# Performance work log

Hardware: AMD Instinct MI355X
Metric: run time of the kernel (lower is better)

## Reference

```python
import jax, jax.numpy as jnp
from jax import lax
import numpy as np

KSIZE = 25  # kernel_size init arg


def _generate_kernel(size):
    center = size // 2
    kernel = np.zeros((size, size), dtype=np.float32)
    for i in range(size):
        if i < center + 1:
            for j in range(size):
                if j < center:
                    kernel[i, j] = j - center - i
                elif j > center:
                    kernel[i, j] = -kernel[i, size - j - 1]
        elif i > center:
            kernel[i, :] = kernel[size - i - 1, :]
    return kernel


def _edge_forward(cube):
    # cube: [B, H, W, C]. Equivalent to the torch block-tiled computation:
    # zero-pad by p, for every interior pixel compute spectral-angle (SAD)
    # between the center spectrum and each pixel of its k x k neighborhood,
    # then 'convolve' (single valid k x k cross-correlation == weighted sum)
    # the SAD patch with fixed gradient kernels Kx / Ky.
    B, H, W, C = cube.shape
    k = KSIZE
    p = k // 2
    Kx = jnp.asarray(_generate_kernel(k))  # [k, k]
    Ky = Kx.T                               # rearrange 'h w -> w h'
    kx_flat = Kx.reshape(-1)
    ky_flat = Ky.reshape(-1)

    padded = jnp.pad(cube, ((0, 0), (p, p), (p, p), (0, 0)))  # [B, H+2p, W+2p, C]
    norm_pad = jnp.sqrt(jnp.sum(padded * padded, axis=-1))    # [B, H+2p, W+2p]
    center = cube                                             # center spectra
    norm_c = norm_pad[:, p:p + H, p:p + W]                    # [B, H, W]

    # Scan over the k*k window offsets; accumulate the two gradient sums
    # without ever materializing the [B,H,W,k,k] SAD volume.
    def step(carry, idx):
        gx, gy = carry
        di, dj = idx // k, idx % k
        shifted = lax.dynamic_slice(padded, (0, di, dj, 0), (B, H, W, C))
        norm_s = lax.dynamic_slice(norm_pad, (0, di, dj), (B, H, W))
        numer = jnp.einsum('bhwc,bhwc->bhw', center, shifted)
        # eps 1e-4 matches torch; tiny clip guards fp32 roundoff past +/-1
        ratio = jnp.clip(numer / (norm_c * norm_s + 1e-4), -1.0 + 1e-6, 1.0 - 1e-6)
        sad = jnp.arccos(ratio)
        return (gx + sad * kx_flat[idx], gy + sad * ky_flat[idx]), None

    init = (jnp.zeros((B, H, W), cube.dtype), jnp.zeros((B, H, W), cube.dtype))
    (gx, gy), _ = lax.scan(jax.checkpoint(step), init, jnp.arange(k * k))
    edge = jnp.abs(gx) + jnp.abs(gy)
    # the torch code zeroes a pad_len border before global-max normalization
    out = jnp.pad(edge[:, p:H - p, p:W - p], ((0, 0), (p, p), (p, p)))
    return out / jnp.max(out)


def setup_inputs() -> dict:
    key = jax.random.key(0)
    cube = jax.random.uniform(key, (1, 400, 400, 128), dtype=jnp.float32)
    return {"cube": cube}


def reference(cube):
    return _edge_forward(cube)
```

## Files before the change

### kernel.cpp

```cpp
#include <hip/hip_runtime.h>
#include <cstdint>
#include <cstddef>


typedef _Float16 half8 __attribute__((ext_vector_type(8)));
typedef float    f32x4 __attribute__((ext_vector_type(4)));

#define HW   400
#define NP   (HW*HW)
#define CCH  128
#define W16  416
#define ROWE (W16*CCH)
#define PAD  12
#define IEND 388


__device__ __forceinline__ float acos_fast(float x) {
  float ax = fabsf(x);
  float s  = __builtin_amdgcn_sqrtf(1.0f - ax);
  float p  = fmaf(ax, -0.0187292994f, 0.0742610134f);
  p = fmaf(p, ax, -0.2121143967f);
  p = fmaf(p, ax,  1.5707287572f);
  float r = s * p;
  return (x >= 0.0f) ? r : (3.14159265359f - r);
}

__global__ void cvt_kernel(const float* __restrict__ cube,
                           _Float16* __restrict__ c16,
                           unsigned* __restrict__ gmax) {
  __shared__ float part[64];
  int pg = blockIdx.x;
  int r  = blockIdx.y;
  int t  = threadIdx.x;
  if (pg == 0 && r == 0 && t == 0) *gmax = 0u;
  int i  = t & 15;
  int q  = (t >> 4) & 3;
  int ks = t >> 6;
  int px = pg*16 + i;
  float v[8];
  if (px < HW) {
    const float* src = cube + ((size_t)(r*HW + px))*CCH + ks*32 + q*8;
    #pragma unroll
    for (int j = 0; j < 8; ++j) v[j] = src[j];
  } else {
    #pragma unroll
    for (int j = 0; j < 8; ++j) v[j] = 0.f;
  }
  float ss = 0.f;
  #pragma unroll
  for (int j = 0; j < 8; ++j) ss += v[j]*v[j];
  ss += __shfl_xor(ss, 16);
  ss += __shfl_xor(ss, 32);
  if (q == 0) part[i*4 + ks] = ss;
  __syncthreads();
  f32x4 pp = *(const f32x4*)&part[i*4];
  float tot = pp.x + pp.y + pp.z + pp.w;
  float sc = (tot > 0.f) ? rsqrtf(tot) : 0.f;
  half8 hv;
  #pragma unroll
  for (int j = 0; j < 8; ++j) hv[j] = (_Float16)(v[j]*sc);
  *(half8*)(c16 + (size_t)r*ROWE + pg*2048 + t*8) = hv;
}

__global__ __launch_bounds__(64, 4) void edge_kernel(
    const _Float16* __restrict__ c16,
    float* __restrict__ gxp, float* __restrict__ gyp) {
  const int id   = blockIdx.x;
  const int g    = (id & 7)*1128 + (id >> 3);
  const int gh   = g / 24;
  const int rem  = g - gh*24;
  const int h    = gh + PAD;
  const int wb   = rem >> 1;
  const int half = rem & 1;
  const int l  = threadIdx.x;
  const int c  = l & 15, q = l >> 4;
  const int w0 = PAD + 32*wb;
  const int g0 = 2*wb;

  half8 A[2][4];
  #pragma unroll
  for (int t = 0; t < 2; ++t) {
    int px = w0 + 16*t + c;
    const _Float16* p = c16 + (size_t)h*ROWE + (px >> 4)*2048 + q*128 + (px & 15)*8;
    #pragma unroll
    for (int ks = 0; ks < 4; ++ks)
      A[t][ks] = *(const half8*)(p + ks*512);
  }

  const float cq = (float)(c - 4*q);

  float gx[2][4], gy[2][4];
  #pragma unroll
  for (int t = 0; t < 2; ++t)
    #pragma unroll
    for (int rr = 0; rr < 4; ++rr) { gx[t][rr] = 0.f; gy[t][rr] = 0.f; }

  const _Float16* bBase = c16 + g0*2048 + (size_t)l*8;
  const int diLo = half ? 13 : 0;
  const int diHi = half ? 25 : 13;

  #pragma unroll 1
  for (int di = diLo; di < diHi; ++di) {
    const int r = h + di - PAD;
    const _Float16* rowB = bBase + (size_t)r*ROWE;

    f32x4 acc[2][3];
    #pragma unroll
    for (int t = 0; t < 2; ++t)
      #pragma unroll
      for (int d = 0; d < 3; ++d) acc[t][d] = (f32x4){0.f,0.f,0.f,0.f};

    #pragma unroll
    for (int ks = 0; ks < 4; ++ks) {
      half8 B0 = *(const half8*)(rowB + 0*2048 + ks*512);
      half8 B1 = *(const half8*)(rowB + 1*2048 + ks*512);
      half8 B2 = *(const half8*)(rowB + 2*2048 + ks*512);
      half8 B3 = *(const half8*)(rowB + 3*2048 + ks*512);
      acc[0][0] = __builtin_amdgcn_mfma_f32_16x16x32_f16(A[0][ks], B0, acc[0][0], 0,0,0);
      acc[0][1] = __builtin_amdgcn_mfma_f32_16x16x32_f16(A[0][ks], B1, acc[0][1], 0,0,0);
      acc[0][2] = __builtin_amdgcn_mfma_f32_16x16x32_f16(A[0][ks], B2, acc[0][2], 0,0,0);
      acc[1][0] = __builtin_amdgcn_mfma_f32_16x16x32_f16(A[1][ks], B1, acc[1][0], 0,0,0);
      acc[1][1] = __builtin_amdgcn_mfma_f32_16x16x32_f16(A[1][ks], B2, acc[1][1], 0,0,0);
      acc[1][2] = __builtin_amdgcn_mfma_f32_16x16x32_f16(A[1][ks], B3, acc[1][2], 0,0,0);
    }

    const float ii  = (float)((di <= 12) ? di : 24 - di);
    const float sdi = (float)((di > 12) - (di < 12));
    const float dif = (float)(di - 12);
    #pragma unroll
    for (int t = 0; t < 2; ++t)
      #pragma unroll
      for (int d = 0; d < 3; ++d)
        #pragma unroll
        for (int rr = 0; rr < 4; ++rr) {
          float p  = cq + (float)(16*d - 12 - rr);
          float ap = fabsf(p);
          float sg = fminf(fmaxf(p, -1.f), 1.f);
          bool  ok = ap <= 12.f;
          float kx = ok ? fmaf(sg, ii, p) : 0.f;
          float ky = ok ? fmaf(sdi, 12.f - ap, dif) : 0.f;
          float ratio = acc[t][d][rr];
          ratio = fminf(fmaxf(ratio, -0.999999f), 0.999999f);
          float sad = acos_fast(ratio);
          gx[t][rr] = fmaf(sad, kx, gx[t][rr]);
          gy[t][rr] = fmaf(sad, ky, gy[t][rr]);
        }
  }

  const int hoff = half*NP + h*HW;
  #pragma unroll
  for (int t = 0; t < 2; ++t)
    #pragma unroll
    for (int rr = 0; rr < 4; ++rr) {
      float sgx = gx[t][rr], sgy = gy[t][rr];
      #pragma unroll
      for (int m = 1; m < 16; m <<= 1) {
        sgx += __shfl_xor(sgx, m);
        sgy += __shfl_xor(sgy, m);
      }
      if (c == rr) {
        int w = w0 + 16*t + 4*q + rr;
        gxp[hoff + w] = sgx;
        gyp[hoff + w] = sgy;
      }
    }
}

__global__ void combine_kernel(float* __restrict__ gxp,
                               const float* __restrict__ gyp,
                               unsigned* __restrict__ gmax) {
  __shared__ float wm[4];
  int idx = blockIdx.x*256 + threadIdx.x;
  int hh = idx / HW;
  int ww = idx - hh*HW;
  float e = 0.f;
  if (hh >= PAD && hh < IEND && ww >= PAD && ww < IEND)
    e = fabsf(gxp[idx] + gxp[NP + idx]) + fabsf(gyp[idx] + gyp[NP + idx]);
  gxp[idx] = e;
  float m = e;
  #pragma unroll
  for (int off = 1; off < 64; off <<= 1) m = fmaxf(m, __shfl_xor(m, off));
  if ((threadIdx.x & 63) == 0) wm[threadIdx.x >> 6] = m;
  __syncthreads();
  if (threadIdx.x == 0) {
    float mm = fmaxf(fmaxf(wm[0], wm[1]), fmaxf(wm[2], wm[3]));
    atomicMax(gmax, __float_as_uint(mm));
  }
}

__global__ void norm_kernel(const float* __restrict__ edge,
                            const unsigned* __restrict__ gmax,
                            float* __restrict__ out) {
  int idx = blockIdx.x*256 + threadIdx.x;
  float mv = __uint_as_float(*gmax);
  out[idx] = edge[idx] / mv;
}

extern "C" void kernel_launch(void* const* d_in, const int* in_sizes, int n_in,
                              void* d_out, int out_size, void* d_ws, size_t ws_size,
                              hipStream_t stream) {
  const float* cube = (const float*)d_in[0];
  char* ws = (char*)d_ws;
  _Float16* c16  = (_Float16*)(ws);
  float*    gxp  = (float*)(ws + 42598400);
  float*    gyp  = (float*)(ws + 42598400 + 8*NP);
  unsigned* gmax = (unsigned*)(ws + 42598400 + 16*NP);

  cvt_kernel<<<dim3(26, 400), 256, 0, stream>>>(cube, c16, gmax);
  edge_kernel<<<9024, 64, 0, stream>>>(c16, gxp, gyp);
  combine_kernel<<<NP/256, 256, 0, stream>>>(gxp, gyp, gmax);
  norm_kernel<<<NP/256, 256, 0, stream>>>(gxp, gmax, (float*)d_out);
}
```

Before: 245.0 us.

## Pack four waves per edge block and hoist kernel-weight math out of inner loop

Each edge-kernel block now holds four wavefronts covering two width tiles and both di halves of one row, with launch bounds raised to 256 threads and 6 blocks per SIMD group. The per-lane Kx/Ky weight setup (masking, sign, abs) is precomputed once into small register arrays, and per-di weights come from two FMAs per entry. The acos clip is folded into a single min on |x|. This cuts VALU work in the hot loop and lets neighbouring waves share B rows in cache, but the extra precomputed arrays add register pressure that could reduce occupancy or cause spills.

```diff
diff --git a/kernel.cpp b/kernel.cpp
--- a/kernel.cpp
+++ b/kernel.cpp
@@ -15,8 +15,8 @@
 #define IEND 388
 
 
-__device__ __forceinline__ float acos_fast(float x) {
-  float ax = fabsf(x);
+__device__ __forceinline__ float acos_clip(float x) {
+  float ax = fminf(fabsf(x), 0.999999f);
   float s  = __builtin_amdgcn_sqrtf(1.0f - ax);
   float p  = fmaf(ax, -0.0187292994f, 0.0742610134f);
   p = fmaf(p, ax, -0.2121143967f);
@@ -62,17 +62,18 @@
   *(half8*)(c16 + (size_t)r*ROWE + pg*2048 + t*8) = hv;
 }
 
-__global__ __launch_bounds__(64, 4) void edge_kernel(
+__global__ __launch_bounds__(256, 6) void edge_kernel(
     const _Float16* __restrict__ c16,
     float* __restrict__ gxp, float* __restrict__ gyp) {
-  const int id   = blockIdx.x;
-  const int g    = (id & 7)*1128 + (id >> 3);
-  const int gh   = g / 24;
-  const int rem  = g - gh*24;
-  const int h    = gh + PAD;
-  const int wb   = rem >> 1;
-  const int half = rem & 1;
-  const int l  = threadIdx.x;
+  const int id  = blockIdx.x;
+  const int g   = (id & 7)*282 + (id >> 3);
+  const int gh  = g / 6;
+  const int sub = g - gh*6;
+  const int h   = gh + PAD;
+  const int wv  = threadIdx.x >> 6;
+  const int l   = threadIdx.x & 63;
+  const int wb   = sub*2 + (wv >> 1);
+  const int half = wv & 1;
   const int c  = l & 15, q = l >> 4;
   const int w0 = PAD + 32*wb;
   const int g0 = 2*wb;
@@ -88,6 +89,20 @@
   }
 
   const float cq = (float)(c - 4*q);
+  float p_m[12], sg_m[12], mn_m[12], one_m[12];
+  #pragma unroll
+  for (int d = 0; d < 3; ++d)
+    #pragma unroll
+    for (int rr = 0; rr < 4; ++rr) {
+      int j = d*4 + rr;
+      float p  = cq + (float)(16*d - 12 - rr);
+      float ap = fabsf(p);
+      bool  ok = ap <= 12.f;
+      p_m[j]  = ok ? p : 0.f;
+      sg_m[j] = ok ? fminf(fmaxf(p, -1.f), 1.f) : 0.f;
+      mn_m[j] = ok ? (12.f - ap) : 0.f;
+      one_m[j]= ok ? 1.f : 0.f;
+    }
 
   float gx[2][4], gy[2][4];
   #pragma unroll
@@ -127,23 +142,23 @@
     const float ii  = (float)((di <= 12) ? di : 24 - di);
     const float sdi = (float)((di > 12) - (di < 12));
     const float dif = (float)(di - 12);
+    float kx[12], ky[12];
+    #pragma unroll
+    for (int j = 0; j < 12; ++j) {
+      kx[j] = fmaf(sg_m[j], ii, p_m[j]);
+      ky[j] = fmaf(sdi, mn_m[j], dif*one_m[j]);
+    }
+
     #pragma unroll
     for (int t = 0; t < 2; ++t)
       #pragma unroll
       for (int d = 0; d < 3; ++d)
         #pragma unroll
         for (int rr = 0; rr < 4; ++rr) {
-          float p  = cq + (float)(16*d - 12 - rr);
-          float ap = fabsf(p);
-          float sg = fminf(fmaxf(p, -1.f), 1.f);
-          bool  ok = ap <= 12.f;
-          float kx = ok ? fmaf(sg, ii, p) : 0.f;
-          float ky = ok ? fmaf(sdi, 12.f - ap, dif) : 0.f;
-          float ratio = acc[t][d][rr];
-          ratio = fminf(fmaxf(ratio, -0.999999f), 0.999999f);
-          float sad = acos_fast(ratio);
-          gx[t][rr] = fmaf(sad, kx, gx[t][rr]);
-          gy[t][rr] = fmaf(sad, ky, gy[t][rr]);
+          int   j   = d*4 + rr;
+          float sad = acos_clip(acc[t][d][rr]);
+          gx[t][rr] = fmaf(sad, kx[j], gx[t][rr]);
+          gy[t][rr] = fmaf(sad, ky[j], gy[t][rr]);
         }
   }
 
@@ -207,7 +222,7 @@
   unsigned* gmax = (unsigned*)(ws + 42598400 + 16*NP);
 
   cvt_kernel<<<dim3(26, 400), 256, 0, stream>>>(cube, c16, gmax);
-  edge_kernel<<<9024, 64, 0, stream>>>(c16, gxp, gyp);
+  edge_kernel<<<2256, 256, 0, stream>>>(c16, gxp, gyp);
   combine_kernel<<<NP/256, 256, 0, stream>>>(gxp, gyp, gmax);
   norm_kernel<<<NP/256, 256, 0, stream>>>(gxp, gmax, (float*)d_out);
 }
```

Measured after the change: 556.3 us. +127.1%, slower.
